# Performance work log

Hardware: AMD Instinct MI355X
Metric: run time of the kernel (lower is better)

Reference implementation:

```python
import jax, jax.numpy as jnp
import numpy as np

TAU = 2.0
ALPHA = 4.0  # spikingjelly surrogate.Sigmoid default
NUM_HEADS = 8


def lif(x, v_th):
    # Multi-step LIF over leading time axis T. v_reset=0, hard reset, tau=2.
    # Forward: Heaviside spike; backward: sigmoid surrogate via straight-through.
    def step(v, xt):
        v = v + (xt - v) / TAU
        hard = (v >= v_th).astype(xt.dtype)
        soft = jax.nn.sigmoid(ALPHA * (v - v_th))
        spike = soft + jax.lax.stop_gradient(hard - soft)
        v = v * (1.0 - jax.lax.stop_gradient(hard))  # detach_reset hard reset to 0
        return v, spike
    _, out = jax.lax.scan(step, jnp.zeros_like(x[0]), x)
    return out


def conv_bn_lif(x, w, scale, bias, v_th=1.0):
    # 1x1 conv (no bias) + folded eval-mode BatchNorm + LIF.
    # x: [T,B,C,H,W], w: [Cout,Cin], scale/bias: [Cout]
    y = jnp.einsum('tbchw,dc->tbdhw', x, w)
    y = y * scale[:, None, None] + bias[:, None, None]
    return lif(y, v_th)


def setup_inputs() -> dict:
    key = jax.random.key(0)
    ks = jax.random.split(key, 14)
    T, B, C, H, W = 4, 32, 384, 14, 14
    x = jax.random.normal(ks[0], (T, B, C, H, W), dtype=jnp.float32)
    def conv_params(k):
        k1, k2, k3 = jax.random.split(k, 3)
        w = jax.random.normal(k1, (C, C), dtype=jnp.float32) * (1.0 / np.sqrt(C))
        scale = jax.random.uniform(k2, (C,), dtype=jnp.float32, minval=0.5, maxval=1.5)
        bias = jax.random.normal(k3, (C,), dtype=jnp.float32) * 0.1
        return w, scale, bias
    wq, sq, bq = conv_params(ks[1])
    wk, sk, bk = conv_params(ks[2])
    wv, sv, bv = conv_params(ks[3])
    wp, sp, bp = conv_params(ks[4])
    return {"x": x, "wq": wq, "sq": sq, "bq": bq, "wk": wk, "sk": sk, "bk": bk,
            "wv": wv, "sv": sv, "bv": bv, "wp": wp, "sp": sp, "bp": bp}


def reference(x, wq, sq, bq, wk, sk, bk, wv, sv, bv, wp, sp, bp):
    T, B, C, H, W = x.shape
    h = NUM_HEADS
    d = C // h
    N = H * W
    # QKV: conv+BN+LIF -> binary spikes [T,B,C,H,W]
    qs = conv_bn_lif(x, wq, sq, bq)
    ks_ = conv_bn_lif(x, wk, sk, bk)
    vs = conv_bn_lif(x, wv, sv, bv)
    # [T,B,C,H,W] -> [T,B,h,d,N] -> [T,B,h,N,d]
    def to_heads(t):
        return t.reshape(T, B, h, d, N).transpose(0, 1, 2, 4, 3)
    q, k, v = to_heads(qs), to_heads(ks_), to_heads(vs)
    attn = jnp.einsum('tbhnd,tbhmd->tbhnm', q, k)
    out = jnp.einsum('tbhnm,tbhmd->tbhnd', attn, v) * 0.125
    out = lif(out, 0.5)  # attn_lif v_threshold=0.5
    # [T,B,h,N,d] -> [T,B,h,d,N] -> [T,B,C,H,W]
    out = out.transpose(0, 1, 2, 4, 3).reshape(T, B, C, H, W)
    out = conv_bn_lif(out, wp, sp, bp)
    return out
```

## Files before the change

kernel.cpp:

```cpp
#include <hip/hip_runtime.h>


#define T_ 4
#define B_ 32
#define C_ 384
#define N_ 196
#define NH_ 8
#define D_ 48
#define TB_ (T_ * B_)
#define CN_ ((size_t)C_ * N_)
#define BCN4_ (B_ * C_ * (N_ / 4))
#define TBCN_ ((size_t)T_ * B_ * C_ * N_)
typedef unsigned long long u64;

__global__ __launch_bounds__(256, 2) void gemm_f32(
    const float* __restrict__ X, const float* __restrict__ W0,
    const float* __restrict__ W1, const float* __restrict__ W2,
    float* __restrict__ P)
{
  const int g = blockIdx.z;
  const float* __restrict__ W = (g == 0) ? W0 : (g == 1) ? W1 : W2;
  const int co0 = blockIdx.y * 128;
  const int j0 = blockIdx.x * 128;
  __shared__ float As[16][128];
  __shared__ float Bs[16][128];
  const int tid = threadIdx.x;
  const int tx = tid & 15, ty = tid >> 4;

  const int bcol = (tid & 31) * 4;
  const int bk = tid >> 5;
  const int bj = j0 + bcol;
  const int btb = bj / N_;
  const float* xb = X + (size_t)btb * CN_ + (bj - btb * N_);
  const int arow = tid >> 1;
  const int ac8 = (tid & 1) * 8;

  float acc[8][8] = {};
  for (int c0 = 0; c0 < C_; c0 += 16) {
    const float* wrow = W + (size_t)(co0 + arow) * C_ + c0 + ac8;
    const float4 a0 = *(const float4*)wrow;
    const float4 a1 = *(const float4*)(wrow + 4);
    As[ac8 + 0][arow] = a0.x; As[ac8 + 1][arow] = a0.y;
    As[ac8 + 2][arow] = a0.z; As[ac8 + 3][arow] = a0.w;
    As[ac8 + 4][arow] = a1.x; As[ac8 + 5][arow] = a1.y;
    As[ac8 + 6][arow] = a1.z; As[ac8 + 7][arow] = a1.w;
    *(float4*)&Bs[bk][bcol]     = *(const float4*)(xb + (size_t)(c0 + bk) * N_);
    *(float4*)&Bs[bk + 8][bcol] = *(const float4*)(xb + (size_t)(c0 + bk + 8) * N_);
    __syncthreads();
#pragma unroll
    for (int k = 0; k < 16; ++k) {
      float a[8], b[8];
      *(float4*)&a[0] = *(const float4*)&As[k][ty * 4];
      *(float4*)&a[4] = *(const float4*)&As[k][64 + ty * 4];
      *(float4*)&b[0] = *(const float4*)&Bs[k][tx * 4];
      *(float4*)&b[4] = *(const float4*)&Bs[k][64 + tx * 4];
#pragma unroll
      for (int i = 0; i < 8; ++i)
#pragma unroll
        for (int j = 0; j < 8; ++j)
          acc[i][j] = fmaf(a[i], b[j], acc[i][j]);
    }
    __syncthreads();
  }
#pragma unroll
  for (int cg = 0; cg < 2; ++cg) {
    const int jj = j0 + cg * 64 + tx * 4;
    const int tb = jj / N_;
    float* pb = P + (size_t)(g * TB_ + tb) * CN_ + (jj - tb * N_);
#pragma unroll
    for (int rg = 0; rg < 2; ++rg) {
#pragma unroll
      for (int i = 0; i < 4; ++i) {
        const int r = rg * 4 + i;
        const int co = co0 + rg * 64 + ty * 4 + i;
        *(float4*)&pb[(size_t)co * N_] = make_float4(
            acc[r][cg * 4 + 0], acc[r][cg * 4 + 1],
            acc[r][cg * 4 + 2], acc[r][cg * 4 + 3]);
      }
    }
  }
}

__global__ __launch_bounds__(256) void lif4(
    const float* __restrict__ In, float* __restrict__ Out,
    const float* __restrict__ s0, const float* __restrict__ b0, float vth)
{
  const long u = (long)blockIdx.x * 256 + threadIdx.x;
  if (u >= BCN4_) return;
  const long r = u;
  const int c = (int)((r / (N_ / 4)) % C_);
  const bool has_bn = (s0 != nullptr);
  const float sc = has_bn ? s0[c] : 1.0f;
  const float bi = has_bn ? b0[c] : 0.0f;
  const float4* In4 = (const float4*)In;
  float4* Out4 = (float4*)Out;
  float v[4] = {0.f, 0.f, 0.f, 0.f};
#pragma unroll
  for (int t = 0; t < T_; ++t) {
    const long idx = (long)t * BCN4_ + r;
    const float4 y4 = In4[idx];
    float y[4] = {y4.x, y4.y, y4.z, y4.w};
    float o[4];
#pragma unroll
    for (int e = 0; e < 4; ++e) {
      const float yb = has_bn ? __fadd_rn(__fmul_rn(y[e], sc), bi) : y[e];
      v[e] = __fadd_rn(v[e], __fmul_rn(__fsub_rn(yb, v[e]), 0.5f));
      const bool fire = (v[e] >= vth);
      o[e] = fire ? 1.0f : 0.0f;
      v[e] = fire ? 0.0f : v[e];
    }
    Out4[idx] = make_float4(o[0], o[1], o[2], o[3]);
  }
}

__global__ __launch_bounds__(1024) void fused_attn(
    const float* __restrict__ P, float* __restrict__ O,
    const float* __restrict__ sq, const float* __restrict__ bq,
    const float* __restrict__ sk, const float* __restrict__ bk,
    const float* __restrict__ sv, const float* __restrict__ bv)
{
  const int h = blockIdx.x;
  const int b = blockIdx.y;
  __shared__ u64 msk[3][T_][D_][4];
  __shared__ float G[D_][52];
  const int tid = threadIdx.x;
  const int wave = tid >> 6, lane = tid & 63;

  for (int task = wave; task < 3 * D_ * 4; task += 16) {
    const int g = task / (D_ * 4);
    const int rem = task - g * (D_ * 4);
    const int j = rem >> 2, w = rem & 3;
    const int m = w * 64 + lane;
    const bool act = (m < N_);
    const int mc = act ? m : (N_ - 1);
    const int c = h * D_ + j;
    const float sc = (g == 0 ? sq : g == 1 ? sk : sv)[c];
    const float bi = (g == 0 ? bq : g == 1 ? bk : bv)[c];
    const float* base = P + (size_t)g * TB_ * CN_ + (size_t)b * CN_
                          + (size_t)c * N_ + mc;
    float v = 0.f;
#pragma unroll
    for (int t = 0; t < T_; ++t) {
      const float y = base[(size_t)t * B_ * CN_];
      const float yb = __fadd_rn(__fmul_rn(y, sc), bi);
      v = __fadd_rn(v, __fmul_rn(__fsub_rn(yb, v), 0.5f));
      const bool fire = (v >= 1.0f);
      if (fire) v = 0.f;
      const u64 bl = __ballot(fire && act);
      if (lane == 0) msk[g][t][j][w] = bl;
    }
  }
  __syncthreads();

  const int u = tid;
  const bool ow = (u < 4 * N_);
  const int dq = ow ? (u / N_) : 0;
  const int n = ow ? (u - dq * N_) : 0;
  const int d0 = dq * 12;
  const int nw = n >> 6, nb = n & 63;
  float vmem[12];
#pragma unroll
  for (int i = 0; i < 12; ++i) vmem[i] = 0.f;

  for (int t = 0; t < T_; ++t) {
    for (int e = tid; e < D_ * D_; e += 1024) {
      const int j = e / D_, d = e - j * D_;
      const u64* kj = msk[1][t][j];
      const u64* vd = msk[2][t][d];
      const int s = __popcll(kj[0] & vd[0]) + __popcll(kj[1] & vd[1]) +
                    __popcll(kj[2] & vd[2]) + __popcll(kj[3] & vd[3]);
      G[j][d] = (float)s;
    }
    __syncthreads();
    if (ow) {
      float out[12];
#pragma unroll
      for (int i = 0; i < 12; ++i) out[i] = 0.f;
#pragma unroll 4
      for (int j = 0; j < D_; ++j) {
        const u64 qw = msk[0][t][j][nw];
        const float qf = (float)((qw >> nb) & 1ull);
        const float* Gj = &G[j][d0];
        const float4 g0 = *(const float4*)&Gj[0];
        const float4 g1 = *(const float4*)&Gj[4];
        const float4 g2 = *(const float4*)&Gj[8];
        out[0] = fmaf(qf, g0.x, out[0]);  out[1] = fmaf(qf, g0.y, out[1]);
        out[2] = fmaf(qf, g0.z, out[2]);  out[3] = fmaf(qf, g0.w, out[3]);
        out[4] = fmaf(qf, g1.x, out[4]);  out[5] = fmaf(qf, g1.y, out[5]);
        out[6] = fmaf(qf, g1.z, out[6]);  out[7] = fmaf(qf, g1.w, out[7]);
        out[8] = fmaf(qf, g2.x, out[8]);  out[9] = fmaf(qf, g2.y, out[9]);
        out[10] = fmaf(qf, g2.z, out[10]); out[11] = fmaf(qf, g2.w, out[11]);
      }
      float* ob = O + ((size_t)(t * B_ + b) * C_ + h * D_ + d0) * N_ + n;
#pragma unroll
      for (int i = 0; i < 12; ++i) {
        const float y = out[i] * 0.125f;
        vmem[i] = __fadd_rn(vmem[i], __fmul_rn(__fsub_rn(y, vmem[i]), 0.5f));
        const bool fire = (vmem[i] >= 0.5f);
        ob[(size_t)i * N_] = fire ? 1.0f : 0.0f;
        if (fire) vmem[i] = 0.f;
      }
    }
    __syncthreads();
  }
}

extern "C" void kernel_launch(void* const* d_in, const int* in_sizes, int n_in,
                              void* d_out, int out_size, void* d_ws, size_t ws_size,
                              hipStream_t stream) {
  const float* x  = (const float*)d_in[0];
  const float* wq = (const float*)d_in[1];
  const float* sq = (const float*)d_in[2];
  const float* bq = (const float*)d_in[3];
  const float* wk = (const float*)d_in[4];
  const float* sk = (const float*)d_in[5];
  const float* bk = (const float*)d_in[6];
  const float* wv = (const float*)d_in[7];
  const float* sv = (const float*)d_in[8];
  const float* bv = (const float*)d_in[9];
  const float* wp = (const float*)d_in[10];
  const float* sp = (const float*)d_in[11];
  const float* bp = (const float*)d_in[12];
  float* out = (float*)d_out;

  float* P = (float*)d_ws;
  float* O = P + 3 * TBCN_;
  float* P2 = P;

  gemm_f32<<<dim3(196, 3, 3), 256, 0, stream>>>(x, wq, wk, wv, P);
  fused_attn<<<dim3(NH_, B_), 1024, 0, stream>>>(P, O, sq, bq, sk, bk, sv, bv);
  gemm_f32<<<dim3(196, 3, 1), 256, 0, stream>>>(O, wp, wp, wp, P2);
  lif4<<<dim3((BCN4_ + 255) / 256), 256, 0, stream>>>(P2, out, sp, bp, 1.0f);
}
```

Before: 540.1 us.

## Bit-slice K^T V Gram matrix and compute Q·G with popcounts

Changes the second attention contraction from float FMAs over a float Gram matrix into bit-plane popcounts. Q spikes are transposed into per-token 48-bit masks, and each K^T V entry, which is at most 196 and so fits in 8 bits, is split into 8 bit-planes via ballots. Each output is then a sum of shifted popcounts. All timesteps are precomputed before the output loop, which removes per-timestep barriers, and the global loads for the LIF scan are batched ahead of the loop. The cost is 8 popcounts per output element plus a bit-transposition pass over Q.

New measurement: 536.4 us. About the same (-0.7%).

```diff
diff --git a/kernel.cpp b/kernel.cpp
--- a/kernel.cpp
+++ b/kernel.cpp
@@ -122,7 +122,8 @@
   const int h = blockIdx.x;
   const int b = blockIdx.y;
   __shared__ u64 msk[3][T_][D_][4];
-  __shared__ float G[D_][52];
+  __shared__ u64 qT[T_][208];
+  __shared__ u64 Gp[T_][8][D_];
   const int tid = threadIdx.x;
   const int wave = tid >> 6, lane = tid & 63;
 
@@ -138,11 +139,13 @@
     const float bi = (g == 0 ? bq : g == 1 ? bk : bv)[c];
     const float* base = P + (size_t)g * TB_ * CN_ + (size_t)b * CN_
                           + (size_t)c * N_ + mc;
+    float y[T_];
+#pragma unroll
+    for (int t = 0; t < T_; ++t) y[t] = base[(size_t)t * B_ * CN_];
     float v = 0.f;
 #pragma unroll
     for (int t = 0; t < T_; ++t) {
-      const float y = base[(size_t)t * B_ * CN_];
-      const float yb = __fadd_rn(__fmul_rn(y, sc), bi);
+      const float yb = __fadd_rn(__fmul_rn(y[t], sc), bi);
       v = __fadd_rn(v, __fmul_rn(__fsub_rn(yb, v), 0.5f));
       const bool fire = (v >= 1.0f);
       if (fire) v = 0.f;
@@ -152,56 +155,55 @@
   }
   __syncthreads();
 
+  {
+    const int t = wave >> 2, w = wave & 3;
+    const int n = w * 64 + lane;
+    u64 qr = 0ull;
+#pragma unroll 8
+    for (int j = 0; j < D_; ++j)
+      qr |= ((msk[0][t][j][w] >> lane) & 1ull) << j;
+    if (n < N_) qT[t][n] = qr;
+  }
+  for (int task = wave; task < T_ * D_; task += 16) {
+    const int t = task / D_, d = task - (task / D_) * D_;
+    const bool ja = (lane < D_);
+    const int j = ja ? lane : (D_ - 1);
+    const u64* kj = msk[1][t][j];
+    const u64* vd = msk[2][t][d];
+    const int gi = __popcll(kj[0] & vd[0]) + __popcll(kj[1] & vd[1]) +
+                   __popcll(kj[2] & vd[2]) + __popcll(kj[3] & vd[3]);
+#pragma unroll
+    for (int p = 0; p < 8; ++p) {
+      const u64 bl = __ballot(ja && ((gi >> p) & 1));
+      if (lane == 0) Gp[t][p][d] = bl;
+    }
+  }
+  __syncthreads();
+
   const int u = tid;
-  const bool ow = (u < 4 * N_);
-  const int dq = ow ? (u / N_) : 0;
-  const int n = ow ? (u - dq * N_) : 0;
-  const int d0 = dq * 12;
-  const int nw = n >> 6, nb = n & 63;
-  float vmem[12];
-#pragma unroll
-  for (int i = 0; i < 12; ++i) vmem[i] = 0.f;
-
-  for (int t = 0; t < T_; ++t) {
-    for (int e = tid; e < D_ * D_; e += 1024) {
-      const int j = e / D_, d = e - j * D_;
-      const u64* kj = msk[1][t][j];
-      const u64* vd = msk[2][t][d];
-      const int s = __popcll(kj[0] & vd[0]) + __popcll(kj[1] & vd[1]) +
-                    __popcll(kj[2] & vd[2]) + __popcll(kj[3] & vd[3]);
-      G[j][d] = (float)s;
-    }
-    __syncthreads();
-    if (ow) {
-      float out[12];
-#pragma unroll
-      for (int i = 0; i < 12; ++i) out[i] = 0.f;
-#pragma unroll 4
-      for (int j = 0; j < D_; ++j) {
-        const u64 qw = msk[0][t][j][nw];
-        const float qf = (float)((qw >> nb) & 1ull);
-        const float* Gj = &G[j][d0];
-        const float4 g0 = *(const float4*)&Gj[0];
-        const float4 g1 = *(const float4*)&Gj[4];
-        const float4 g2 = *(const float4*)&Gj[8];
-        out[0] = fmaf(qf, g0.x, out[0]);  out[1] = fmaf(qf, g0.y, out[1]);
-        out[2] = fmaf(qf, g0.z, out[2]);  out[3] = fmaf(qf, g0.w, out[3]);
-        out[4] = fmaf(qf, g1.x, out[4]);  out[5] = fmaf(qf, g1.y, out[5]);
-        out[6] = fmaf(qf, g1.z, out[6]);  out[7] = fmaf(qf, g1.w, out[7]);
-        out[8] = fmaf(qf, g2.x, out[8]);  out[9] = fmaf(qf, g2.y, out[9]);
-        out[10] = fmaf(qf, g2.z, out[10]); out[11] = fmaf(qf, g2.w, out[11]);
-      }
+  if (u < 4 * N_) {
+    const int dq = u / N_;
+    const int n = u - dq * N_;
+    const int d0 = dq * 12;
+    float vmem[12];
+#pragma unroll
+    for (int i = 0; i < 12; ++i) vmem[i] = 0.f;
+    for (int t = 0; t < T_; ++t) {
+      const u64 qr = qT[t][n];
       float* ob = O + ((size_t)(t * B_ + b) * C_ + h * D_ + d0) * N_ + n;
 #pragma unroll
       for (int i = 0; i < 12; ++i) {
-        const float y = out[i] * 0.125f;
+        int acc = 0;
+#pragma unroll
+        for (int p = 0; p < 8; ++p)
+          acc += __popcll(qr & Gp[t][p][d0 + i]) << p;
+        const float y = __int2float_rn(acc) * 0.125f;
         vmem[i] = __fadd_rn(vmem[i], __fmul_rn(__fsub_rn(y, vmem[i]), 0.5f));
         const bool fire = (vmem[i] >= 0.5f);
         ob[(size_t)i * N_] = fire ? 1.0f : 0.0f;
         if (fire) vmem[i] = 0.f;
       }
     }
-    __syncthreads();
   }
 }
 
```
